# Performance work log

Hardware: AMD Instinct MI355X
Metric: run time of the kernel (lower is better)

## Reference

```python
import jax, jax.numpy as jnp
import numpy as np

GROUPS = 32
EPS = 1e-5


def group_norm(x, gamma, beta):
    b, h, w, c = x.shape
    xg = x.reshape(b, h, w, GROUPS, c // GROUPS)
    mean = jnp.mean(xg, axis=(1, 2, 4), keepdims=True)
    var = jnp.var(xg, axis=(1, 2, 4), keepdims=True)
    xn = ((xg - mean) * jax.lax.rsqrt(var + EPS)).reshape(b, h, w, c)
    return xn * gamma + beta


def conv1x1(x, w, b):
    # 1x1 conv == per-pixel dense: [b,h,w,c] x [c,d] -> [b,h,w,d]
    return jnp.einsum('bhwc,cd->bhwd', x, w) + b


def setup_inputs() -> dict:
    key = jax.random.key(0)
    ks = jax.random.split(key, 6)
    B, H, W, C = 4, 64, 64, 512
    s = 1.0 / np.sqrt(C)
    return {
        'x': jax.random.normal(ks[0], (B, H, W, C), jnp.float32),
        'gn_gamma': jnp.ones((C,), jnp.float32),
        'gn_beta': jnp.zeros((C,), jnp.float32),
        'wq': jax.random.normal(ks[1], (C, C), jnp.float32) * s,
        'bq': jnp.zeros((C,), jnp.float32),
        'wk': jax.random.normal(ks[2], (C, C), jnp.float32) * s,
        'bk': jnp.zeros((C,), jnp.float32),
        'wv': jax.random.normal(ks[3], (C, C), jnp.float32) * s,
        'bv': jnp.zeros((C,), jnp.float32),
        'wp': jax.random.normal(ks[4], (C, C), jnp.float32) * s,
        'bp': jnp.zeros((C,), jnp.float32),
    }


def reference(x, gn_gamma, gn_beta, wq, bq, wk, bk, wv, bv, wp, bp):
    b, h, w, c = x.shape
    n = h * w
    h_ = group_norm(x, gn_gamma, gn_beta)
    q = conv1x1(h_, wq, bq).reshape(b, n, c)
    k = conv1x1(h_, wk, bk).reshape(b, n, c)
    v = conv1x1(h_, wv, bv).reshape(b, n, c)
    scale = c ** (-0.5)
    scores = jnp.einsum('bic,bjc->bij', q, k) * scale  # [b, n, n]
    attn = jax.nn.softmax(scores, axis=-1)
    out = jnp.einsum('bij,bjc->bic', attn, v).reshape(b, h, w, c)
    return x + conv1x1(out, wp, bp)
```

## Files before the change

kernel.cpp:

```cpp
#include <hip/hip_runtime.h>
#include <cstdint>


typedef __bf16 bf16_t;
typedef bf16_t bf16x8 __attribute__((ext_vector_type(8)));
typedef float floatx4 __attribute__((ext_vector_type(4)));
typedef int v8i __attribute__((ext_vector_type(8)));

__device__ __forceinline__ uint16_t f2b(float f) {
    uint32_t u = __builtin_bit_cast(uint32_t, f);
    u += 0x7fffu + ((u >> 16) & 1u);
    return (uint16_t)(u >> 16);
}
__device__ __forceinline__ float b2f(uint16_t h) {
    uint32_t u = ((uint32_t)h) << 16;
    return __builtin_bit_cast(float, u);
}
__device__ __forceinline__ unsigned pk_fp8x4(float a, float b, float c, float d) {
    int w = __builtin_amdgcn_cvt_pk_fp8_f32(a, b, 0, false);
    w = __builtin_amdgcn_cvt_pk_fp8_f32(c, d, w, true);
    return (unsigned)w;
}

__device__ __forceinline__ void lds_copy16(void* lds, const void* glob) {
    __builtin_amdgcn_global_load_lds(
        (__attribute__((address_space(1))) void*)(void*)glob,
        (__attribute__((address_space(3))) void*)lds,
        16, 0, 0);
}

__global__ __launch_bounds__(256) void gn_stats(const float* __restrict__ x,
                                                float* __restrict__ stats) {
    const int bg = blockIdx.x;
    const int tid = threadIdx.x;
    const int b = bg >> 5, g = bg & 31;
    const float* base = x + (long)b * (4096L * 512) + g * 16;
    float s = 0.f, sq = 0.f;
    #pragma unroll 8
    for (int i = 0; i < 64; i++) {
        int idx4 = tid + i * 256;
        int pixel = idx4 >> 2, c4 = idx4 & 3;
        const float4 v = *(const float4*)(base + (long)pixel * 512 + c4 * 4);
        s += v.x + v.y + v.z + v.w;
        sq += v.x * v.x + v.y * v.y + v.z * v.z + v.w * v.w;
    }
    #pragma unroll
    for (int off = 32; off > 0; off >>= 1) {
        s += __shfl_down(s, off);
        sq += __shfl_down(sq, off);
    }
    __shared__ float rs[4], rq[4];
    const int lane = tid & 63, w = tid >> 6;
    if (lane == 0) { rs[w] = s; rq[w] = sq; }
    __syncthreads();
    if (tid == 0) {
        float S = rs[0] + rs[1] + rs[2] + rs[3];
        float Q = rq[0] + rq[1] + rq[2] + rq[3];
        float mean = S * (1.f / 65536.f);
        float var = Q * (1.f / 65536.f) - mean * mean;
        stats[bg * 2 + 0] = mean;
        stats[bg * 2 + 1] = rsqrtf(var + 1e-5f);
    }
}

__global__ __launch_bounds__(256) void gn_apply(const float* __restrict__ x,
                                                const float* __restrict__ stats,
                                                const float* __restrict__ gamma,
                                                const float* __restrict__ beta,
                                                uint16_t* __restrict__ h) {
    const long idx4 = (long)blockIdx.x * 256 + threadIdx.x;
    const long e0 = idx4 * 4;
    const int c = (int)(e0 & 511);
    const int b = (int)(e0 >> 21);
    const float2 st = ((const float2*)stats)[b * 32 + (c >> 4)];
    const float4 v = ((const float4*)x)[idx4];
    const float4 gm = ((const float4*)gamma)[c >> 2];
    const float4 bt = ((const float4*)beta)[c >> 2];
    union { ushort4 u; uint16_t s[4]; } o;
    o.s[0] = f2b((v.x - st.x) * st.y * gm.x + bt.x);
    o.s[1] = f2b((v.y - st.x) * st.y * gm.y + bt.y);
    o.s[2] = f2b((v.z - st.x) * st.y * gm.z + bt.z);
    o.s[3] = f2b((v.w - st.x) * st.y * gm.w + bt.w);
    ((ushort4*)h)[idx4] = o.u;
}

__global__ __launch_bounds__(256) void wcast_transpose(const float* __restrict__ w0,
                                                       const float* __restrict__ w1,
                                                       const float* __restrict__ w2,
                                                       const float* __restrict__ w3,
                                                       uint16_t* __restrict__ out) {
    const float* ws[4] = {w0, w1, w2, w3};
    const float* w = ws[blockIdx.z];
    uint16_t* o = out + (long)blockIdx.z * 512 * 512;
    __shared__ uint16_t t[64][65];
    const int nb = blockIdx.x * 64, kb = blockIdx.y * 64;
    const int lc = threadIdx.x & 63, lg = threadIdx.x >> 6;
    #pragma unroll
    for (int i = 0; i < 16; i++) {
        int r = lg * 16 + i;
        t[lc][r] = f2b(w[(long)(kb + r) * 512 + nb + lc]);
    }
    __syncthreads();
    #pragma unroll
    for (int i = 0; i < 16; i++) {
        int r = lg * 16 + i;
        o[(long)(nb + r) * 512 + kb + lc] = t[r][lc];
    }
}

__global__ __launch_bounds__(256) void qkv_gemm(const uint16_t* __restrict__ h,
                                                const uint16_t* __restrict__ wT,
                                                const float* __restrict__ bq,
                                                const float* __restrict__ bk,
                                                const float* __restrict__ bv,
                                                uint8_t* __restrict__ q,
                                                uint8_t* __restrict__ k,
                                                uint8_t* __restrict__ vt) {
    __shared__ __align__(16) uint16_t smem[128 * 136];
    uint16_t* sA = smem;
    uint16_t* sB = smem + 8192;

    const int tid = threadIdx.x;
    const long m0 = (long)blockIdx.y * 128;
    const int n0 = blockIdx.x * 128;

    const int lane = tid & 63;
    const int wave = tid >> 6;
    const int wm = (wave & 1) * 64;
    const int wn = (wave >> 1) * 64;
    const int fr = lane & 15;
    const int fh = lane >> 4;
    const int sw = fr & 7;

    floatx4 acc[4][4];
    #pragma unroll
    for (int i = 0; i < 4; i++)
        #pragma unroll
        for (int j = 0; j < 4; j++) acc[i][j] = (floatx4){0.f, 0.f, 0.f, 0.f};

    for (int kt = 0; kt < 512; kt += 64) {
        __syncthreads();
        #pragma unroll
        for (int i = 0; i < 4; i++) {
            const int c = i * 256 + tid;
            const int row = c >> 3;
            const int gj = (c & 7) ^ (row & 7);
            lds_copy16(&sA[c * 8], h + (m0 + row) * 512L + kt + gj * 8);
            lds_copy16(&sB[c * 8], wT + (n0 + row) * 512L + kt + gj * 8);
        }
        __syncthreads();
        #pragma unroll
        for (int kk = 0; kk < 64; kk += 32) {
            const int jx = ((fh + (kk >> 3)) ^ sw) * 8;
            bf16x8 av[4], bv_[4];
            #pragma unroll
            for (int mi = 0; mi < 4; mi++)
                av[mi] = *(const bf16x8*)&sA[(wm + mi * 16 + fr) * 64 + jx];
            #pragma unroll
            for (int ni = 0; ni < 4; ni++)
                bv_[ni] = *(const bf16x8*)&sB[(wn + ni * 16 + fr) * 64 + jx];
            #pragma unroll
            for (int mi = 0; mi < 4; mi++)
                #pragma unroll
                for (int ni = 0; ni < 4; ni++)
                    acc[mi][ni] = __builtin_amdgcn_mfma_f32_16x16x32_bf16(
                        av[mi], bv_[ni], acc[mi][ni], 0, 0, 0);
        }
    }

    const int quad = lane >> 4;
    const int w = n0 >> 9;
    const int nc = n0 & 511;
    const float* bias = (w == 0) ? bq : (w == 1) ? bk : bv;
    __syncthreads();
    if (w < 2) {
        #pragma unroll
        for (int ni = 0; ni < 4; ni++) {
            const int col_l = wn + ni * 16 + fr;
            const float bb = bias[nc + col_l];
            #pragma unroll
            for (int mi = 0; mi < 4; mi++) {
                #pragma unroll
                for (int r = 0; r < 4; r++) {
                    const int row_l = wm + mi * 16 + quad * 4 + r;
                    smem[row_l * 136 + col_l] = f2b(acc[mi][ni][r] + bb);
                }
            }
        }
        __syncthreads();
        uint8_t* out = (w == 0) ? q : k;
        #pragma unroll
        for (int it = 0; it < 8; it++) {
            const int row_l = it * 16 + (tid >> 4);
            const int c0 = (tid & 15) * 8;
            const uint4 d = *(const uint4*)&smem[row_l * 136 + c0];
            const uint16_t* e = (const uint16_t*)&d;
            uint2 o;
            o.x = pk_fp8x4(b2f(e[0]), b2f(e[1]), b2f(e[2]), b2f(e[3]));
            o.y = pk_fp8x4(b2f(e[4]), b2f(e[5]), b2f(e[6]), b2f(e[7]));
            *(uint2*)&out[(m0 + row_l) * 512 + nc + c0] = o;
        }
    } else {
        uint8_t* s8 = (uint8_t*)smem;
        #pragma unroll
        for (int ni = 0; ni < 4; ni++) {
            const int ch_l = wn + ni * 16 + fr;
            const float bb = bias[nc + ch_l];
            #pragma unroll
            for (int mi = 0; mi < 4; mi++) {
                const int pix0 = wm + mi * 16 + quad * 4;
                *(unsigned*)&s8[ch_l * 144 + pix0] =
                    pk_fp8x4(acc[mi][ni][0] + bb, acc[mi][ni][1] + bb,
                             acc[mi][ni][2] + bb, acc[mi][ni][3] + bb);
            }
        }
        __syncthreads();
        const long b = m0 >> 12;
        const int pixb = (int)(m0 & 4095);
        uint8_t* vtb = vt + b * (512L * 4096);
        #pragma unroll
        for (int it = 0; it < 4; it++) {
            const int ch_l = it * 32 + (tid >> 3);
            const int p0 = (tid & 7) * 16;
            *(uint4*)&vtb[(long)(nc + ch_l) * 4096 + pixb + p0] =
                *(const uint4*)&s8[ch_l * 144 + p0];
        }
    }
}

__global__ __launch_bounds__(512, 2) void flash_attn(const uint8_t* __restrict__ q8,
                                                     const uint8_t* __restrict__ k8,
                                                     const uint8_t* __restrict__ vt8,
                                                     uint16_t* __restrict__ ao) {
    __shared__ __align__(16) uint8_t sK[65536];
    __shared__ __align__(16) uint8_t Pl[64 * 128];
    __shared__ float lpart[8][16];
    __shared__ float linv[64];
    __shared__ __align__(16) uint16_t obuf[64 * 256];

    const int tid = threadIdx.x;
    const int lane = tid & 63;
    const int wave = tid >> 6;
    const int fr = lane & 15;
    const int quad = lane >> 4;
    const int sw = fr & 7;

    const int lb = ((blockIdx.x & 7) << 5) | (blockIdx.x >> 3);
    const int batch = lb >> 6;
    const int mt = lb & 63;
    const long qbase = (long)batch * 4096 + mt * 64;

    const int wm = (wave >> 1) * 16;
    const int wc = (wave & 1) * 64;
    const float qscale = 0.06375871540654937f;

    v8i aQ[4];
    {
        const uint8_t* qp = q8 + (qbase + wm + fr) * 512 + quad * 32;
        #pragma unroll
        for (int kt = 0; kt < 4; kt++) {
            const uint4 lo = *(const uint4*)(qp + kt * 128);
            const uint4 hi = *(const uint4*)(qp + kt * 128 + 16);
            aQ[kt] = (v8i){(int)lo.x, (int)lo.y, (int)lo.z, (int)lo.w,
                           (int)hi.x, (int)hi.y, (int)hi.z, (int)hi.w};
        }
    }
    const uint8_t* kbb = k8 + (long)batch * (4096L * 512);
    const uint8_t* vrow = vt8 + (long)batch * (512L * 4096) +
                          (long)(wave * 64 + fr) * 4096 + quad * 32;

    floatx4 oacc[4][4];
    #pragma unroll
    for (int i = 0; i < 4; i++)
        #pragma unroll
        for (int j = 0; j < 4; j++) oacc[i][j] = (floatx4){0.f, 0.f, 0.f, 0.f};
    float lsum[4] = {0.f, 0.f, 0.f, 0.f};

    for (int t = 0; t < 32; t++) {
        __syncthreads();
        {
            const uint8_t* kb = kbb + (long)t * (128L * 512);
            #pragma unroll
            for (int i = 0; i < 8; i++) {
                const int chunk = i * 512 + tid;
                const int kt = chunk >> 10;
                const int c = chunk & 1023;
                const int row = c >> 3;
                const int gj = (c & 7) ^ (row & 7);
                lds_copy16(&sK[kt * 16384 + c * 16],
                           kb + row * 512 + kt * 128 + gj * 16);
            }
        }
        __syncthreads();
        v8i bV[4];
        #pragma unroll
        for (int ni = 0; ni < 4; ni++) {
            const uint8_t* vp = vrow + (long)ni * (16L * 4096) + t * 128;
            const uint4 lo = *(const uint4*)vp;
            const uint4 hi = *(const uint4*)(vp + 16);
            bV[ni] = (v8i){(int)lo.x, (int)lo.y, (int)lo.z, (int)lo.w,
                           (int)hi.x, (int)hi.y, (int)hi.z, (int)hi.w};
        }
        floatx4 sacc[4];
        #pragma unroll
        for (int ni = 0; ni < 4; ni++) sacc[ni] = (floatx4){0.f, 0.f, 0.f, 0.f};
        #pragma unroll
        for (int kt = 0; kt < 4; kt++) {
            v8i bK[4];
            #pragma unroll
            for (int ni = 0; ni < 4; ni++) {
                const int row = wc + ni * 16 + fr;
                const uint8_t* base = &sK[kt * 16384 + row * 128];
                const uint4 lo = *(const uint4*)(base + (((2 * quad) ^ sw) << 4));
                const uint4 hi = *(const uint4*)(base + (((2 * quad + 1) ^ sw) << 4));
                bK[ni] = (v8i){(int)lo.x, (int)lo.y, (int)lo.z, (int)lo.w,
                               (int)hi.x, (int)hi.y, (int)hi.z, (int)hi.w};
            }
            #pragma unroll
            for (int ni = 0; ni < 4; ni++)
                sacc[ni] = __builtin_amdgcn_mfma_scale_f32_16x16x128_f8f6f4(
                    aQ[kt], bK[ni], sacc[ni], 0, 0, 0, 0x7f7f7f7fu, 0,
                    0x7f7f7f7fu);
        }
        unsigned pk[4];
        #pragma unroll
        for (int ni = 0; ni < 4; ni++) {
            const float p0 = exp2f(sacc[ni][0] * qscale);
            const float p1 = exp2f(sacc[ni][1] * qscale);
            const float p2 = exp2f(sacc[ni][2] * qscale);
            const float p3 = exp2f(sacc[ni][3] * qscale);
            lsum[0] += p0;
            lsum[1] += p1;
            lsum[2] += p2;
            lsum[3] += p3;
            pk[ni] = pk_fp8x4(p0, p1, p2, p3);
        }
        #pragma unroll
        for (int ni = 0; ni < 4; ni++) {
            const int chunk = ((wave & 1) << 2) | ni;
            #pragma unroll
            for (int r = 0; r < 4; r++) {
                const int prow = wm + quad * 4 + r;
                Pl[prow * 128 + ((chunk ^ (prow & 7)) << 4) + fr] =
                    (uint8_t)(pk[ni] >> (8 * r));
            }
        }
        __syncthreads();
        #pragma unroll
        for (int mi = 0; mi < 4; mi++) {
            const int prow = mi * 16 + fr;
            const uint4 lo = *(const uint4*)&Pl[prow * 128 + (((2 * quad) ^ sw) << 4)];
            const uint4 hi = *(const uint4*)&Pl[prow * 128 + (((2 * quad + 1) ^ sw) << 4)];
            const v8i aP = (v8i){(int)lo.x, (int)lo.y, (int)lo.z, (int)lo.w,
                                 (int)hi.x, (int)hi.y, (int)hi.z, (int)hi.w};
            #pragma unroll
            for (int ni = 0; ni < 4; ni++)
                oacc[mi][ni] = __builtin_amdgcn_mfma_scale_f32_16x16x128_f8f6f4(
                    aP, bV[ni], oacc[mi][ni], 0, 0, 0, 0x7f7f7f7fu, 0,
                    0x7f7f7f7fu);
        }
    }

    #pragma unroll
    for (int r = 0; r < 4; r++) {
        #pragma unroll
        for (int off = 1; off < 16; off <<= 1)
            lsum[r] += __shfl_xor(lsum[r], off);
    }
    if ((lane & 15) == 0) {
        #pragma unroll
        for (int r = 0; r < 4; r++) lpart[wave][quad * 4 + r] = lsum[r];
    }
    __syncthreads();
    if (tid < 64) {
        const int j = tid >> 4;
        const float L = lpart[2 * j][tid & 15] + lpart[2 * j + 1][tid & 15];
        linv[tid] = __builtin_amdgcn_rcpf(L);
    }
    __syncthreads();
    #pragma unroll
    for (int hh = 0; hh < 2; hh++) {
        if ((wave >> 2) == hh) {
            #pragma unroll
            for (int mi = 0; mi < 4; mi++)
                #pragma unroll
                for (int ni = 0; ni < 4; ni++)
                    #pragma unroll
                    for (int r = 0; r < 4; r++) {
                        const int row = mi * 16 + quad * 4 + r;
                        const int col = (wave & 3) * 64 + ni * 16 + fr;
                        obuf[row * 256 + col] = f2b(oacc[mi][ni][r] * linv[row]);
                    }
        }
        __syncthreads();
        {
            const int srow = tid >> 3;
            const int sc = tid & 7;
            uint16_t* dst = ao + (qbase + srow) * 512 + hh * 256;
            const uint16_t* src = &obuf[srow * 256];
            #pragma unroll
            for (int it = 0; it < 4; it++)
                *(uint4*)(dst + (sc + it * 8) * 8) =
                    *(const uint4*)(src + (sc + it * 8) * 8);
        }
        __syncthreads();
    }
}

__global__ __launch_bounds__(256) void gemm_proj(const uint16_t* __restrict__ A,
                                                 const uint16_t* __restrict__ B,
                                                 float* __restrict__ Cout,
                                                 const float* __restrict__ bias,
                                                 const float* __restrict__ resid) {
    __shared__ __align__(16) uint16_t smem[128 * 136];
    uint16_t* sA = smem;
    uint16_t* sB = smem + 8192;
    const int N = 512;

    const int tid = threadIdx.x;
    const long m0 = (long)blockIdx.y * 128;
    const long n0 = (long)blockIdx.x * 128;

    const int lane = tid & 63;
    const int wave = tid >> 6;
    const int wm = (wave & 1) * 64;
    const int wn = (wave >> 1) * 64;
    const int fr = lane & 15;
    const int fh = lane >> 4;
    const int sw = fr & 7;

    floatx4 acc[4][4];
    #pragma unroll
    for (int i = 0; i < 4; i++)
        #pragma unroll
        for (int j = 0; j < 4; j++) acc[i][j] = (floatx4){0.f, 0.f, 0.f, 0.f};

    for (int kt = 0; kt < 512; kt += 64) {
        __syncthreads();
        #pragma unroll
        for (int i = 0; i < 4; i++) {
            const int c = i * 256 + tid;
            const int row = c >> 3;
            const int gj = (c & 7) ^ (row & 7);
            lds_copy16(&sA[c * 8], A + (m0 + row) * 512L + kt + gj * 8);
            lds_copy16(&sB[c * 8], B + (n0 + row) * 512L + kt + gj * 8);
        }
        __syncthreads();
        #pragma unroll
        for (int kk = 0; kk < 64; kk += 32) {
            const int jx = ((fh + (kk >> 3)) ^ sw) * 8;
            bf16x8 av[4], bv[4];
            #pragma unroll
            for (int mi = 0; mi < 4; mi++)
                av[mi] = *(const bf16x8*)&sA[(wm + mi * 16 + fr) * 64 + jx];
            #pragma unroll
            for (int ni = 0; ni < 4; ni++)
                bv[ni] = *(const bf16x8*)&sB[(wn + ni * 16 + fr) * 64 + jx];
            #pragma unroll
            for (int mi = 0; mi < 4; mi++)
                #pragma unroll
                for (int ni = 0; ni < 4; ni++)
                    acc[mi][ni] = __builtin_amdgcn_mfma_f32_16x16x32_bf16(
                        av[mi], bv[ni], acc[mi][ni], 0, 0, 0);
        }
    }

    const int quad = lane >> 4;
    #pragma unroll
    for (int ni = 0; ni < 4; ni++) {
        const long col = n0 + wn + ni * 16 + fr;
        const float bv_ = bias[col];
        #pragma unroll
        for (int mi = 0; mi < 4; mi++) {
            #pragma unroll
            for (int r = 0; r < 4; r++) {
                const long row = m0 + wm + mi * 16 + quad * 4 + r;
                Cout[row * N + col] = acc[mi][ni][r] + bv_ + resid[row * N + col];
            }
        }
    }
}

extern "C" void kernel_launch(void* const* d_in, const int* in_sizes, int n_in,
                              void* d_out, int out_size, void* d_ws, size_t ws_size,
                              hipStream_t stream) {
    const float* x  = (const float*)d_in[0];
    const float* gg = (const float*)d_in[1];
    const float* gb = (const float*)d_in[2];
    const float* wq = (const float*)d_in[3];
    const float* bq = (const float*)d_in[4];
    const float* wk = (const float*)d_in[5];
    const float* bk = (const float*)d_in[6];
    const float* wv = (const float*)d_in[7];
    const float* bv = (const float*)d_in[8];
    const float* wp = (const float*)d_in[9];
    const float* bp = (const float*)d_in[10];
    float* out = (float*)d_out;

    char* ws = (char*)d_ws;
    size_t off = 0;
    auto alloc = [&](size_t bytes) {
        char* p = ws + off;
        off += (bytes + 255) & ~(size_t)255;
        return p;
    };
    float*    stats = (float*)alloc(128 * 2 * sizeof(float));
    uint16_t* h     = (uint16_t*)alloc(16384L * 512 * 2);
    uint16_t* wT    = (uint16_t*)alloc(4L * 512 * 512 * 2);
    uint8_t*  q8    = (uint8_t*)alloc(16384L * 512);
    uint8_t*  k8    = (uint8_t*)alloc(16384L * 512);
    uint8_t*  vt8   = (uint8_t*)alloc(16384L * 512);
    uint16_t* ao    = (uint16_t*)alloc(16384L * 512 * 2);
    if (off > ws_size) return;

    gn_stats<<<128, 256, 0, stream>>>(x, stats);
    gn_apply<<<8192, 256, 0, stream>>>(x, stats, gg, gb, h);
    wcast_transpose<<<dim3(8, 8, 4), 256, 0, stream>>>(wq, wk, wv, wp, wT);

    qkv_gemm<<<dim3(12, 128), 256, 0, stream>>>(h, wT, bq, bk, bv, q8, k8, vt8);
    flash_attn<<<dim3(256), dim3(512), 0, stream>>>(q8, k8, vt8, ao);
    gemm_proj<<<dim3(4, 128), 256, 0, stream>>>(ao, wT + 3 * 262144, out, bp, x);
}
```

Baseline: 318.1 us.

## Double-buffer K tiles in LDS and retile QK waves to 32x32

The K tile is now double-buffered in LDS: the next tile's async copy is issued right after the top-of-loop barrier, so it overlaps the current tile's QK and PV MFMAs, and one barrier per iteration goes away. The output staging buffer now reuses the K LDS space. The QK^T wave tiling changes from 16 rows by 64 columns to 32 by 32, which halves per-wave K fragment reads from LDS but doubles the Q registers held. The row-sum reduction is updated to match. LDS use per block rises to roughly 138KB, and register pressure goes up.

New measurement: 321.4 us. About the same (+1.1%).

```diff
diff --git a/kernel.cpp b/kernel.cpp
--- a/kernel.cpp
+++ b/kernel.cpp
@@ -232,11 +232,11 @@
                                                      const uint8_t* __restrict__ k8,
                                                      const uint8_t* __restrict__ vt8,
                                                      uint16_t* __restrict__ ao) {
-    __shared__ __align__(16) uint8_t sK[65536];
-    __shared__ __align__(16) uint8_t Pl[64 * 128];
-    __shared__ float lpart[8][16];
+    __shared__ __align__(16) uint8_t sK[2][65536];
+    __shared__ __align__(16) uint8_t Pl[8192];
+    __shared__ float lpart[8][32];
     __shared__ float linv[64];
-    __shared__ __align__(16) uint16_t obuf[64 * 256];
+    uint16_t* obuf = (uint16_t*)sK;
 
     const int tid = threadIdx.x;
     const int lane = tid & 63;
@@ -250,19 +250,22 @@
     const int mt = lb & 63;
     const long qbase = (long)batch * 4096 + mt * 64;
 
-    const int wm = (wave >> 1) * 16;
-    const int wc = (wave & 1) * 64;
+    const int wr = wave >> 2;
+    const int wcg = wave & 3;
+    const int wm = wr * 32;
+    const int wc = wcg * 32;
     const float qscale = 0.06375871540654937f;
 
-    v8i aQ[4];
-    {
-        const uint8_t* qp = q8 + (qbase + wm + fr) * 512 + quad * 32;
+    v8i aQ[2][4];
+    #pragma unroll
+    for (int mi = 0; mi < 2; mi++) {
+        const uint8_t* qp = q8 + (qbase + wm + mi * 16 + fr) * 512 + quad * 32;
         #pragma unroll
         for (int kt = 0; kt < 4; kt++) {
             const uint4 lo = *(const uint4*)(qp + kt * 128);
             const uint4 hi = *(const uint4*)(qp + kt * 128 + 16);
-            aQ[kt] = (v8i){(int)lo.x, (int)lo.y, (int)lo.z, (int)lo.w,
-                           (int)hi.x, (int)hi.y, (int)hi.z, (int)hi.w};
+            aQ[mi][kt] = (v8i){(int)lo.x, (int)lo.y, (int)lo.z, (int)lo.w,
+                               (int)hi.x, (int)hi.y, (int)hi.z, (int)hi.w};
         }
     }
     const uint8_t* kbb = k8 + (long)batch * (4096L * 512);
@@ -274,23 +277,32 @@
     for (int i = 0; i < 4; i++)
         #pragma unroll
         for (int j = 0; j < 4; j++) oacc[i][j] = (floatx4){0.f, 0.f, 0.f, 0.f};
-    float lsum[4] = {0.f, 0.f, 0.f, 0.f};
+    float lsum[2][4];
+    #pragma unroll
+    for (int i = 0; i < 2; i++)
+        #pragma unroll
+        for (int r = 0; r < 4; r++) lsum[i][r] = 0.f;
+
+#define STAGE(t_, buf_)                                                        \
+    do {                                                                       \
+        const uint8_t* kb = kbb + (long)(t_) * (128L * 512);                   \
+        uint8_t* dst = &sK[buf_][0];                                           \
+        _Pragma("unroll")                                                      \
+        for (int i = 0; i < 8; i++) {                                          \
+            const int chunk = i * 512 + tid;                                   \
+            const int kt = chunk >> 10;                                        \
+            const int c = chunk & 1023;                                        \
+            const int row = c >> 3;                                            \
+            const int gj = (c & 7) ^ (row & 7);                                \
+            lds_copy16(dst + kt * 16384 + c * 16,                              \
+                       kb + row * 512 + kt * 128 + gj * 16);                   \
+        }                                                                      \
+    } while (0)
+
+    STAGE(0, 0);
 
     for (int t = 0; t < 32; t++) {
-        __syncthreads();
-        {
-            const uint8_t* kb = kbb + (long)t * (128L * 512);
-            #pragma unroll
-            for (int i = 0; i < 8; i++) {
-                const int chunk = i * 512 + tid;
-                const int kt = chunk >> 10;
-                const int c = chunk & 1023;
-                const int row = c >> 3;
-                const int gj = (c & 7) ^ (row & 7);
-                lds_copy16(&sK[kt * 16384 + c * 16],
-                           kb + row * 512 + kt * 128 + gj * 16);
-            }
-        }
+        const int cur = t & 1;
         __syncthreads();
         v8i bV[4];
         #pragma unroll
@@ -301,48 +313,52 @@
             bV[ni] = (v8i){(int)lo.x, (int)lo.y, (int)lo.z, (int)lo.w,
                            (int)hi.x, (int)hi.y, (int)hi.z, (int)hi.w};
         }
-        floatx4 sacc[4];
-        #pragma unroll
-        for (int ni = 0; ni < 4; ni++) sacc[ni] = (floatx4){0.f, 0.f, 0.f, 0.f};
+        if (t < 31) STAGE(t + 1, cur ^ 1);
+        floatx4 sacc[2][2];
+        #pragma unroll
+        for (int mi = 0; mi < 2; mi++)
+            #pragma unroll
+            for (int ni = 0; ni < 2; ni++) sacc[mi][ni] = (floatx4){0.f, 0.f, 0.f, 0.f};
         #pragma unroll
         for (int kt = 0; kt < 4; kt++) {
-            v8i bK[4];
-            #pragma unroll
-            for (int ni = 0; ni < 4; ni++) {
+            v8i bK[2];
+            #pragma unroll
+            for (int ni = 0; ni < 2; ni++) {
                 const int row = wc + ni * 16 + fr;
-                const uint8_t* base = &sK[kt * 16384 + row * 128];
+                const uint8_t* base = &sK[cur][kt * 16384 + row * 128];
                 const uint4 lo = *(const uint4*)(base + (((2 * quad) ^ sw) << 4));
                 const uint4 hi = *(const uint4*)(base + (((2 * quad + 1) ^ sw) << 4));
                 bK[ni] = (v8i){(int)lo.x, (int)lo.y, (int)lo.z, (int)lo.w,
                                (int)hi.x, (int)hi.y, (int)hi.z, (int)hi.w};
             }
             #pragma unroll
-            for (int ni = 0; ni < 4; ni++)
-                sacc[ni] = __builtin_amdgcn_mfma_scale_f32_16x16x128_f8f6f4(
-                    aQ[kt], bK[ni], sacc[ni], 0, 0, 0, 0x7f7f7f7fu, 0,
-                    0x7f7f7f7fu);
-        }
-        unsigned pk[4];
-        #pragma unroll
-        for (int ni = 0; ni < 4; ni++) {
-            const float p0 = exp2f(sacc[ni][0] * qscale);
-            const float p1 = exp2f(sacc[ni][1] * qscale);
-            const float p2 = exp2f(sacc[ni][2] * qscale);
-            const float p3 = exp2f(sacc[ni][3] * qscale);
-            lsum[0] += p0;
-            lsum[1] += p1;
-            lsum[2] += p2;
-            lsum[3] += p3;
-            pk[ni] = pk_fp8x4(p0, p1, p2, p3);
-        }
-        #pragma unroll
-        for (int ni = 0; ni < 4; ni++) {
-            const int chunk = ((wave & 1) << 2) | ni;
-            #pragma unroll
-            for (int r = 0; r < 4; r++) {
-                const int prow = wm + quad * 4 + r;
-                Pl[prow * 128 + ((chunk ^ (prow & 7)) << 4) + fr] =
-                    (uint8_t)(pk[ni] >> (8 * r));
+            for (int mi = 0; mi < 2; mi++)
+                #pragma unroll
+                for (int ni = 0; ni < 2; ni++)
+                    sacc[mi][ni] = __builtin_amdgcn_mfma_scale_f32_16x16x128_f8f6f4(
+                        aQ[mi][kt], bK[ni], sacc[mi][ni], 0, 0, 0, 0x7f7f7f7fu, 0,
+                        0x7f7f7f7fu);
+        }
+        #pragma unroll
+        for (int mi = 0; mi < 2; mi++) {
+            #pragma unroll
+            for (int ni = 0; ni < 2; ni++) {
+                const float p0 = exp2f(sacc[mi][ni][0] * qscale);
+                const float p1 = exp2f(sacc[mi][ni][1] * qscale);
+                const float p2 = exp2f(sacc[mi][ni][2] * qscale);
+                const float p3 = exp2f(sacc[mi][ni][3] * qscale);
+                lsum[mi][0] += p0;
+                lsum[mi][1] += p1;
+                lsum[mi][2] += p2;
+                lsum[mi][3] += p3;
+                const unsigned pw = pk_fp8x4(p0, p1, p2, p3);
+                const int chunk = wcg * 2 + ni;
+                #pragma unroll
+                for (int r = 0; r < 4; r++) {
+                    const int prow = wm + mi * 16 + quad * 4 + r;
+                    Pl[prow * 128 + ((chunk ^ (prow & 7)) << 4) + fr] =
+                        (uint8_t)(pw >> (8 * r));
+                }
             }
         }
         __syncthreads();
@@ -360,21 +376,28 @@
                     0x7f7f7f7fu);
         }
     }
-
-    #pragma unroll
-    for (int r = 0; r < 4; r++) {
-        #pragma unroll
-        for (int off = 1; off < 16; off <<= 1)
-            lsum[r] += __shfl_xor(lsum[r], off);
-    }
+#undef STAGE
+
+    #pragma unroll
+    for (int mi = 0; mi < 2; mi++)
+        #pragma unroll
+        for (int r = 0; r < 4; r++) {
+            #pragma unroll
+            for (int off = 1; off < 16; off <<= 1)
+                lsum[mi][r] += __shfl_xor(lsum[mi][r], off);
+        }
     if ((lane & 15) == 0) {
         #pragma unroll
-        for (int r = 0; r < 4; r++) lpart[wave][quad * 4 + r] = lsum[r];
+        for (int mi = 0; mi < 2; mi++)
+            #pragma unroll
+            for (int r = 0; r < 4; r++)
+                lpart[wave][mi * 16 + quad * 4 + r] = lsum[mi][r];
     }
     __syncthreads();
     if (tid < 64) {
-        const int j = tid >> 4;
-        const float L = lpart[2 * j][tid & 15] + lpart[2 * j + 1][tid & 15];
+        const int wr_ = tid >> 5, rl = tid & 31;
+        const float L = lpart[wr_ * 4 + 0][rl] + lpart[wr_ * 4 + 1][rl] +
+                        lpart[wr_ * 4 + 2][rl] + lpart[wr_ * 4 + 3][rl];
         linv[tid] = __builtin_amdgcn_rcpf(L);
     }
     __syncthreads();
```

## Halve flash-attention query tile to 32 rows, doubling grid and occupancy

Applied to the files above, without the earlier changes.

Each flash-attention block now handles 32 query rows instead of 64, so the grid grows from 256 to 512 blocks and launch bounds request 4 blocks per CU. The wave layout changes to 2 row groups by 4 column groups of 32 keys. The output staging buffer now aliases the K shared-memory tile, which cuts LDS use, and the V loads are issued after the QK MFMAs. The aim is to fill the 256 CUs better and hide latency, at the cost of loading each K/V tile twice as often and doing less MFMA work per K load.

Result: slower. 418.5 us (+31.6%).

```diff
diff --git a/kernel.cpp b/kernel.cpp
--- a/kernel.cpp
+++ b/kernel.cpp
@@ -228,15 +228,15 @@
     }
 }
 
-__global__ __launch_bounds__(512, 2) void flash_attn(const uint8_t* __restrict__ q8,
+__global__ __launch_bounds__(512, 4) void flash_attn(const uint8_t* __restrict__ q8,
                                                      const uint8_t* __restrict__ k8,
                                                      const uint8_t* __restrict__ vt8,
                                                      uint16_t* __restrict__ ao) {
     __shared__ __align__(16) uint8_t sK[65536];
-    __shared__ __align__(16) uint8_t Pl[64 * 128];
+    __shared__ __align__(16) uint8_t Pl[4096];
     __shared__ float lpart[8][16];
-    __shared__ float linv[64];
-    __shared__ __align__(16) uint16_t obuf[64 * 256];
+    __shared__ float linv[32];
+    uint16_t* obuf = (uint16_t*)sK;
 
     const int tid = threadIdx.x;
     const int lane = tid & 63;
@@ -245,13 +245,15 @@
     const int quad = lane >> 4;
     const int sw = fr & 7;
 
-    const int lb = ((blockIdx.x & 7) << 5) | (blockIdx.x >> 3);
-    const int batch = lb >> 6;
-    const int mt = lb & 63;
-    const long qbase = (long)batch * 4096 + mt * 64;
-
-    const int wm = (wave >> 1) * 16;
-    const int wc = (wave & 1) * 64;
+    const int lb = ((blockIdx.x & 7) << 6) | (blockIdx.x >> 3);
+    const int batch = lb >> 7;
+    const int mt = lb & 127;
+    const long qbase = (long)batch * 4096 + mt * 32;
+
+    const int wr = wave >> 2;
+    const int wcg = wave & 3;
+    const int wm = wr * 16;
+    const int wc = wcg * 32;
     const float qscale = 0.06375871540654937f;
 
     v8i aQ[4];
@@ -269,9 +271,9 @@
     const uint8_t* vrow = vt8 + (long)batch * (512L * 4096) +
                           (long)(wave * 64 + fr) * 4096 + quad * 32;
 
-    floatx4 oacc[4][4];
-    #pragma unroll
-    for (int i = 0; i < 4; i++)
+    floatx4 oacc[2][4];
+    #pragma unroll
+    for (int i = 0; i < 2; i++)
         #pragma unroll
         for (int j = 0; j < 4; j++) oacc[i][j] = (floatx4){0.f, 0.f, 0.f, 0.f};
     float lsum[4] = {0.f, 0.f, 0.f, 0.f};
@@ -292,6 +294,27 @@
             }
         }
         __syncthreads();
+        floatx4 sacc[2];
+        #pragma unroll
+        for (int ni = 0; ni < 2; ni++) sacc[ni] = (floatx4){0.f, 0.f, 0.f, 0.f};
+        #pragma unroll
+        for (int kt = 0; kt < 4; kt++) {
+            v8i bK[2];
+            #pragma unroll
+            for (int ni = 0; ni < 2; ni++) {
+                const int row = wc + ni * 16 + fr;
+                const uint8_t* base = &sK[kt * 16384 + row * 128];
+                const uint4 lo = *(const uint4*)(base + (((2 * quad) ^ sw) << 4));
+                const uint4 hi = *(const uint4*)(base + (((2 * quad + 1) ^ sw) << 4));
+                bK[ni] = (v8i){(int)lo.x, (int)lo.y, (int)lo.z, (int)lo.w,
+                               (int)hi.x, (int)hi.y, (int)hi.z, (int)hi.w};
+            }
+            #pragma unroll
+            for (int ni = 0; ni < 2; ni++)
+                sacc[ni] = __builtin_amdgcn_mfma_scale_f32_16x16x128_f8f6f4(
+                    aQ[kt], bK[ni], sacc[ni], 0, 0, 0, 0x7f7f7f7fu, 0,
+                    0x7f7f7f7fu);
+        }
         v8i bV[4];
         #pragma unroll
         for (int ni = 0; ni < 4; ni++) {
@@ -301,30 +324,8 @@
             bV[ni] = (v8i){(int)lo.x, (int)lo.y, (int)lo.z, (int)lo.w,
                            (int)hi.x, (int)hi.y, (int)hi.z, (int)hi.w};
         }
-        floatx4 sacc[4];
-        #pragma unroll
-        for (int ni = 0; ni < 4; ni++) sacc[ni] = (floatx4){0.f, 0.f, 0.f, 0.f};
-        #pragma unroll
-        for (int kt = 0; kt < 4; kt++) {
-            v8i bK[4];
-            #pragma unroll
-            for (int ni = 0; ni < 4; ni++) {
-                const int row = wc + ni * 16 + fr;
-                const uint8_t* base = &sK[kt * 16384 + row * 128];
-                const uint4 lo = *(const uint4*)(base + (((2 * quad) ^ sw) << 4));
-                const uint4 hi = *(const uint4*)(base + (((2 * quad + 1) ^ sw) << 4));
-                bK[ni] = (v8i){(int)lo.x, (int)lo.y, (int)lo.z, (int)lo.w,
-                               (int)hi.x, (int)hi.y, (int)hi.z, (int)hi.w};
-            }
-            #pragma unroll
-            for (int ni = 0; ni < 4; ni++)
-                sacc[ni] = __builtin_amdgcn_mfma_scale_f32_16x16x128_f8f6f4(
-                    aQ[kt], bK[ni], sacc[ni], 0, 0, 0, 0x7f7f7f7fu, 0,
-                    0x7f7f7f7fu);
-        }
-        unsigned pk[4];
-        #pragma unroll
-        for (int ni = 0; ni < 4; ni++) {
+        #pragma unroll
+        for (int ni = 0; ni < 2; ni++) {
             const float p0 = exp2f(sacc[ni][0] * qscale);
             const float p1 = exp2f(sacc[ni][1] * qscale);
             const float p2 = exp2f(sacc[ni][2] * qscale);
@@ -333,21 +334,18 @@
             lsum[1] += p1;
             lsum[2] += p2;
             lsum[3] += p3;
-            pk[ni] = pk_fp8x4(p0, p1, p2, p3);
-        }
-        #pragma unroll
-        for (int ni = 0; ni < 4; ni++) {
-            const int chunk = ((wave & 1) << 2) | ni;
+            const unsigned pw = pk_fp8x4(p0, p1, p2, p3);
+            const int chunk = wcg * 2 + ni;
             #pragma unroll
             for (int r = 0; r < 4; r++) {
                 const int prow = wm + quad * 4 + r;
                 Pl[prow * 128 + ((chunk ^ (prow & 7)) << 4) + fr] =
-                    (uint8_t)(pk[ni] >> (8 * r));
-            }
-        }
-        __syncthreads();
-        #pragma unroll
-        for (int mi = 0; mi < 4; mi++) {
+                    (uint8_t)(pw >> (8 * r));
+            }
+        }
+        __syncthreads();
+        #pragma unroll
+        for (int mi = 0; mi < 2; mi++) {
             const int prow = mi * 16 + fr;
             const uint4 lo = *(const uint4*)&Pl[prow * 128 + (((2 * quad) ^ sw) << 4)];
             const uint4 hi = *(const uint4*)&Pl[prow * 128 + (((2 * quad + 1) ^ sw) << 4)];
@@ -372,38 +370,33 @@
         for (int r = 0; r < 4; r++) lpart[wave][quad * 4 + r] = lsum[r];
     }
     __syncthreads();
-    if (tid < 64) {
-        const int j = tid >> 4;
-        const float L = lpart[2 * j][tid & 15] + lpart[2 * j + 1][tid & 15];
+    if (tid < 32) {
+        const int wr_ = tid >> 4, rl = tid & 15;
+        const float L = lpart[wr_ * 4 + 0][rl] + lpart[wr_ * 4 + 1][rl] +
+                        lpart[wr_ * 4 + 2][rl] + lpart[wr_ * 4 + 3][rl];
         linv[tid] = __builtin_amdgcn_rcpf(L);
     }
     __syncthreads();
     #pragma unroll
-    for (int hh = 0; hh < 2; hh++) {
-        if ((wave >> 2) == hh) {
-            #pragma unroll
-            for (int mi = 0; mi < 4; mi++)
-                #pragma unroll
-                for (int ni = 0; ni < 4; ni++)
-                    #pragma unroll
-                    for (int r = 0; r < 4; r++) {
-                        const int row = mi * 16 + quad * 4 + r;
-                        const int col = (wave & 3) * 64 + ni * 16 + fr;
-                        obuf[row * 256 + col] = f2b(oacc[mi][ni][r] * linv[row]);
-                    }
-        }
-        __syncthreads();
-        {
-            const int srow = tid >> 3;
-            const int sc = tid & 7;
-            uint16_t* dst = ao + (qbase + srow) * 512 + hh * 256;
-            const uint16_t* src = &obuf[srow * 256];
-            #pragma unroll
-            for (int it = 0; it < 4; it++)
-                *(uint4*)(dst + (sc + it * 8) * 8) =
-                    *(const uint4*)(src + (sc + it * 8) * 8);
-        }
-        __syncthreads();
+    for (int mi = 0; mi < 2; mi++)
+        #pragma unroll
+        for (int ni = 0; ni < 4; ni++)
+            #pragma unroll
+            for (int r = 0; r < 4; r++) {
+                const int row = mi * 16 + quad * 4 + r;
+                const int col = wave * 64 + ni * 16 + fr;
+                obuf[row * 512 + col] = f2b(oacc[mi][ni][r] * linv[row]);
+            }
+    __syncthreads();
+    {
+        const int srow = tid >> 4;
+        const int sc = tid & 15;
+        uint16_t* dst = ao + (qbase + srow) * 512;
+        const uint16_t* src = &obuf[srow * 512];
+        #pragma unroll
+        for (int it = 0; it < 4; it++)
+            *(uint4*)(dst + (sc + it * 16) * 8) =
+                *(const uint4*)(src + (sc + it * 16) * 8);
     }
 }
 
@@ -518,6 +511,6 @@
     wcast_transpose<<<dim3(8, 8, 4), 256, 0, stream>>>(wq, wk, wv, wp, wT);
 
     qkv_gemm<<<dim3(12, 128), 256, 0, stream>>>(h, wT, bq, bk, bv, q8, k8, vt8);
-    flash_attn<<<dim3(256), dim3(512), 0, stream>>>(q8, k8, vt8, ao);
+    flash_attn<<<dim3(512), dim3(512), 0, stream>>>(q8, k8, vt8, ao);
     gemm_proj<<<dim3(4, 128), 256, 0, stream>>>(ao, wT + 3 * 262144, out, bp, x);
 }
```
